# Performance work log

Measured on AMD Instinct MI355X. Metric: run time of the kernel, lower is better.

## Reference

```python
import jax, jax.numpy as jnp
import numpy as np

TEMP = 1.0
EPS = 1e-15

B, N, F, K = 8, 2000, 128, 64


def setup_inputs() -> dict:
    key = jax.random.key(0)
    k1, k2, k3 = jax.random.split(key, 3)
    x = jax.random.normal(k1, (B, N, F), dtype=jnp.float32)
    adj = jax.random.uniform(k2, (B, N, N), dtype=jnp.float32)
    s = jax.random.normal(k3, (B, N, K), dtype=jnp.float32)
    mask = jnp.ones((B, N), dtype=bool)
    return {"x": x, "adj": adj, "s": s, "mask": mask}


def reference(x, adj, s, mask):
    k = s.shape[-1]
    s = jax.nn.softmax(s / TEMP, axis=-1)
    m = mask[..., None].astype(x.dtype)          # [B,N,1]
    x = x * m
    s = s * m

    # pooled features: s^T x -> [B,K,F]
    out = jnp.einsum('bnk,bnf->bkf', s, x)

    # pooled adjacency: s^T A s -> [B,K,K]
    as_ = jnp.einsum('bnm,bmk->bnk', adj, s)     # A s, [B,N,K]
    out_adj = jnp.einsum('bnk,bnl->bkl', as_, s)

    # mincut loss
    mincut_num = jnp.einsum('bkk->b', out_adj)
    d_flat = jnp.sum(adj, axis=-1)               # degree, [B,N]
    # trace(s^T diag(d) s) = sum_n d_n * sum_k s_nk^2 (avoids dense diag)
    mincut_den = jnp.einsum('bn,bnk,bnk->b', d_flat, s, s)
    mincut_loss = jnp.mean(-(mincut_num / mincut_den))

    # orthogonality loss
    ss = jnp.einsum('bnk,bnl->bkl', s, s)        # [B,K,K]
    ss_norm = jnp.linalg.norm(ss, axis=(-2, -1), keepdims=True)
    i_s = jnp.eye(k, dtype=ss.dtype)
    ortho = jnp.linalg.norm(ss / ss_norm - i_s / jnp.sqrt(jnp.asarray(k, ss.dtype)), axis=(-2, -1))
    ortho_loss = jnp.mean(ortho)

    # zero diagonal, symmetric degree normalization
    ind = jnp.arange(k)
    out_adj = out_adj.at[:, ind, ind].set(0.0)
    d = jnp.sqrt(jnp.sum(out_adj, axis=-1))[:, None, :] + EPS  # [B,1,K]
    out_adj = out_adj / d / jnp.swapaxes(d, 1, 2)

    return out, out_adj, mincut_loss, ortho_loss
```

## Files before the change

### kernel.cpp

```cpp
#include <hip/hip_runtime.h>

typedef __bf16 bf16;
typedef __bf16 bf16x8 __attribute__((ext_vector_type(8)));
typedef float f32x4 __attribute__((ext_vector_type(4)));
typedef float f32x16 __attribute__((ext_vector_type(16)));

#define NB 8
#define NN 2000
#define N2 2048
#define KK 64
#define FF 128

__global__ __launch_bounds__(256) void k1_softmax(const float* __restrict__ s,
                                                  bf16* __restrict__ sT,
                                                  float* __restrict__ rowsq) {
  const int b = blockIdx.x >> 5, tile = blockIdx.x & 31;
  const int n0 = tile * 64;
  const int t = threadIdx.x;
  const int r = t >> 2, q = t & 3;
  __shared__ float ptile[64][65];
  const int n = n0 + r;
  const bool valid = n < NN;
  float v[16];
  if (valid) {
    const float4* src = (const float4*)(s + ((size_t)(b * NN + n)) * KK + q * 16);
#pragma unroll
    for (int i = 0; i < 4; ++i) {
      float4 f = src[i];
      v[4 * i + 0] = f.x; v[4 * i + 1] = f.y; v[4 * i + 2] = f.z; v[4 * i + 3] = f.w;
    }
  } else {
#pragma unroll
    for (int i = 0; i < 16; ++i) v[i] = 0.f;
  }
  float mx = v[0];
#pragma unroll
  for (int i = 1; i < 16; ++i) mx = fmaxf(mx, v[i]);
  mx = fmaxf(mx, __shfl_xor(mx, 1));
  mx = fmaxf(mx, __shfl_xor(mx, 2));
  float sum = 0.f;
#pragma unroll
  for (int i = 0; i < 16; ++i) { v[i] = __expf(v[i] - mx); sum += v[i]; }
  sum += __shfl_xor(sum, 1);
  sum += __shfl_xor(sum, 2);
  const float scale = valid ? (1.0f / sum) : 0.f;
  float rq = 0.f;
#pragma unroll
  for (int i = 0; i < 16; ++i) { v[i] *= scale; rq += v[i] * v[i]; }
  rq += __shfl_xor(rq, 1);
  rq += __shfl_xor(rq, 2);
  if (q == 0) rowsq[b * N2 + n0 + r] = rq;
#pragma unroll
  for (int i = 0; i < 16; ++i) ptile[r][q * 16 + i] = v[i];
  __syncthreads();
  bf16x8 o0, o1;
#pragma unroll
  for (int i = 0; i < 8; ++i) o0[i] = (bf16)ptile[q * 16 + i][r];
#pragma unroll
  for (int i = 0; i < 8; ++i) o1[i] = (bf16)ptile[q * 16 + 8 + i][r];
  bf16* dst = sT + ((size_t)(b * KK + r)) * N2 + n0 + q * 16;
  *(bf16x8*)dst = o0;
  *(bf16x8*)(dst + 8) = o1;
}

__global__ __launch_bounds__(256) void k1b_xt(const float* __restrict__ x,
                                              bf16* __restrict__ xT) {
  const int b = blockIdx.x >> 5, tile = blockIdx.x & 31;
  const int n0 = tile * 64;
  const int t = threadIdx.x;
  __shared__ float xt[64 * 132];
#pragma unroll
  for (int i = 0; i < 8; ++i) {
    int idx = t + 256 * i;
    int row = idx >> 5, c4 = idx & 31;
    int n = n0 + row;
    float4 vv = make_float4(0.f, 0.f, 0.f, 0.f);
    if (n < NN) vv = ((const float4*)(x + ((size_t)(b * NN + n)) * FF))[c4];
    *(float4*)&xt[row * 132 + c4 * 4] = vv;
  }
  __syncthreads();
  const int f = t >> 1, h = t & 1;
  bf16* dst = xT + ((size_t)(b * FF + f)) * N2 + n0 + h * 32;
#pragma unroll
  for (int g = 0; g < 4; ++g) {
    bf16x8 o;
#pragma unroll
    for (int i = 0; i < 8; ++i) o[i] = (bf16)xt[(h * 32 + g * 8 + i) * 132 + f];
    *(bf16x8*)(dst + g * 8) = o;
  }
}

__global__ __launch_bounds__(256) void k2_adjs(const float* __restrict__ adj,
                                               const bf16* __restrict__ sT,
                                               bf16* __restrict__ asT) {
  const int b = blockIdx.x >> 5, tile = blockIdx.x & 31;
  const int n0 = tile * 64;
  const int t = threadIdx.x;
  const int w = t >> 6, l = t & 63;
  const int lr = l & 15, lq = l >> 4;
  __shared__ bf16 aT[64 * 72];
  __shared__ bf16 sTl[64 * 72];
  f32x4 acc[4];
#pragma unroll
  for (int ct = 0; ct < 4; ++ct)
#pragma unroll
    for (int rr = 0; rr < 4; ++rr) acc[ct][rr] = 0.f;
  const int r = t >> 2, q = t & 3;
  const bool rowok = (n0 + r) < NN;
  const float* adjrow = adj + ((size_t)b * NN + (rowok ? (n0 + r) : 0)) * NN;
  const bf16* srow = sT + ((size_t)(b * KK + r)) * N2;
  for (int m0 = 0; m0 < N2; m0 += 64) {
    float fv[16];
#pragma unroll
    for (int i = 0; i < 4; ++i) {
      int m = m0 + q * 16 + i * 4;
      float4 f = make_float4(0.f, 0.f, 0.f, 0.f);
      if (rowok && m < NN) f = *(const float4*)(adjrow + m);
      fv[4 * i + 0] = f.x; fv[4 * i + 1] = f.y; fv[4 * i + 2] = f.z; fv[4 * i + 3] = f.w;
    }
    bf16x8 c0, c1;
#pragma unroll
    for (int i = 0; i < 8; ++i) { c0[i] = (bf16)fv[i]; c1[i] = (bf16)fv[8 + i]; }
    *(bf16x8*)&aT[r * 72 + q * 16] = c0;
    *(bf16x8*)&aT[r * 72 + q * 16 + 8] = c1;
    const bf16x8* sp = (const bf16x8*)(srow + m0 + q * 16);
    *(bf16x8*)&sTl[r * 72 + q * 16] = sp[0];
    *(bf16x8*)&sTl[r * 72 + q * 16 + 8] = sp[1];
    __syncthreads();
#pragma unroll
    for (int ks = 0; ks < 2; ++ks) {
      const int mo = ks * 32 + lq * 8;
      bf16x8 af = *(const bf16x8*)&aT[(w * 16 + lr) * 72 + mo];
#pragma unroll
      for (int ct = 0; ct < 4; ++ct) {
        bf16x8 bfv = *(const bf16x8*)&sTl[(ct * 16 + lr) * 72 + mo];
        acc[ct] = __builtin_amdgcn_mfma_f32_16x16x32_bf16(af, bfv, acc[ct], 0, 0, 0);
      }
    }
    __syncthreads();
  }
#pragma unroll
  for (int ct = 0; ct < 4; ++ct)
#pragma unroll
    for (int rr = 0; rr < 4; ++rr)
      aT[(ct * 16 + lr) * 72 + (w * 16 + lq * 4 + rr)] = (bf16)acc[ct][rr];
  __syncthreads();
  bf16* dst = asT + ((size_t)(b * KK + r)) * N2 + n0 + q * 16;
  *(bf16x8*)dst = *(const bf16x8*)&aT[r * 72 + q * 16];
  *(bf16x8*)(dst + 8) = *(const bf16x8*)&aT[r * 72 + q * 16 + 8];
}

__global__ __launch_bounds__(256) void k2b_den(const bf16* __restrict__ asT,
                                               const float* __restrict__ rowsq,
                                               float* __restrict__ den_part) {
  const int b = blockIdx.x >> 3, c = blockIdx.x & 7;
  const int t = threadIdx.x;
  const int n = c * 256 + t;
  const bf16* base = asT + (size_t)b * KK * N2 + n;
  float dsum = 0.f;
#pragma unroll 8
  for (int kk = 0; kk < KK; ++kk) dsum += (float)base[(size_t)kk * N2];
  float val = dsum * rowsq[b * N2 + n];
  __shared__ float red[256];
  red[t] = val;
  __syncthreads();
  for (int s2 = 128; s2 > 0; s2 >>= 1) {
    if (t < s2) red[t] += red[t + s2];
    __syncthreads();
  }
  if (t == 0) den_part[b * 8 + c] = red[0];
}

__global__ __launch_bounds__(256) void k3_gemms(const bf16* __restrict__ sT,
                                                const bf16* __restrict__ asT,
                                                const bf16* __restrict__ xT,
                                                float* __restrict__ adjraw,
                                                float* __restrict__ ssw,
                                                float* __restrict__ dout) {
  const int b = blockIdx.x >> 4, tile = blockIdx.x & 15;
  const bf16 *Ab, *Bb;
  float* Cb;
  int ldC, row0, col0;
  if (tile < 4) {
    int rt = tile >> 1, ct = tile & 1;
    Ab = asT + ((size_t)(b * KK + rt * 32)) * N2;
    Bb = sT + ((size_t)(b * KK + ct * 32)) * N2;
    Cb = adjraw + b * KK * KK; ldC = KK; row0 = rt * 32; col0 = ct * 32;
  } else if (tile < 8) {
    int u = tile - 4; int rt = u >> 1, ct = u & 1;
    Ab = sT + ((size_t)(b * KK + rt * 32)) * N2;
    Bb = sT + ((size_t)(b * KK + ct * 32)) * N2;
    Cb = ssw + b * KK * KK; ldC = KK; row0 = rt * 32; col0 = ct * 32;
  } else {
    int u = tile - 8; int rt = u >> 2, ct = u & 3;
    Ab = sT + ((size_t)(b * KK + rt * 32)) * N2;
    Bb = xT + ((size_t)(b * FF + ct * 32)) * N2;
    Cb = dout + b * KK * FF; ldC = FF; row0 = rt * 32; col0 = ct * 32;
  }
  const int t = threadIdx.x;
  const int w = t >> 6, l = t & 63;
  __shared__ bf16 At[32 * 72];
  __shared__ bf16 Bt[32 * 72];
  __shared__ float Ct[4 * 32 * 33];
  const int srow = t >> 3, sseg = t & 7;
  f32x16 acc;
#pragma unroll
  for (int i = 0; i < 16; ++i) acc[i] = 0.f;
  for (int m0 = 0; m0 < N2; m0 += 64) {
    *(bf16x8*)&At[srow * 72 + sseg * 8] = *(const bf16x8*)(Ab + (size_t)srow * N2 + m0 + sseg * 8);
    *(bf16x8*)&Bt[srow * 72 + sseg * 8] = *(const bf16x8*)(Bb + (size_t)srow * N2 + m0 + sseg * 8);
    __syncthreads();
    const int mo = w * 16 + (l >> 5) * 8;
    bf16x8 af = *(const bf16x8*)&At[(l & 31) * 72 + mo];
    bf16x8 bfv = *(const bf16x8*)&Bt[(l & 31) * 72 + mo];
    acc = __builtin_amdgcn_mfma_f32_32x32x16_bf16(af, bfv, acc, 0, 0, 0);
    __syncthreads();
  }
#pragma unroll
  for (int rr = 0; rr < 16; ++rr) {
    int row = (rr & 3) + 8 * (rr >> 2) + 4 * (l >> 5);
    Ct[(w * 32 + row) * 33 + (l & 31)] = acc[rr];
  }
  __syncthreads();
#pragma unroll
  for (int i = 0; i < 4; ++i) {
    int e = t + 256 * i;
    int row = e >> 5, col = e & 31;
    float v = Ct[row * 33 + col] + Ct[(32 + row) * 33 + col] +
              Ct[(64 + row) * 33 + col] + Ct[(96 + row) * 33 + col];
    Cb[(size_t)(row0 + row) * ldC + col0 + col] = v;
  }
}

__device__ inline float wred64(float v) {
#pragma unroll
  for (int off = 32; off > 0; off >>= 1) v += __shfl_xor(v, off);
  return v;
}

__global__ __launch_bounds__(64) void k4_final(const float* __restrict__ adjraw,
                                               const float* __restrict__ ssw,
                                               const float* __restrict__ den_part,
                                               float* __restrict__ dout,
                                               float* __restrict__ loss_part) {
  const int b = blockIdx.x;
  const int lane = threadIdx.x;
  float den = 0.f;
#pragma unroll
  for (int c = 0; c < 8; ++c) den += den_part[b * 8 + c];
  const float* arow = adjraw + b * 4096 + lane * 64;
  float4 av[16];
#pragma unroll
  for (int i = 0; i < 16; ++i) av[i] = ((const float4*)arow)[i];
  const float diag = adjraw[b * 4096 + lane * 65];
  float rs = 0.f;
#pragma unroll
  for (int i = 0; i < 16; ++i) rs += av[i].x + av[i].y + av[i].z + av[i].w;
  rs -= diag;
  const float num = wred64(diag);
  const float d = sqrtf(rs) + 1e-15f;
  __shared__ float dsh[64];
  dsh[lane] = d;
  __syncthreads();
  const float invd = 1.0f / d;
  float* orow = dout + NB * KK * FF + b * 4096 + lane * 64;
#pragma unroll
  for (int i = 0; i < 16; ++i) {
    float4 cvv = av[i];
    cvv.x = (4 * i + 0 == lane) ? 0.f : cvv.x * invd / dsh[4 * i + 0];
    cvv.y = (4 * i + 1 == lane) ? 0.f : cvv.y * invd / dsh[4 * i + 1];
    cvv.z = (4 * i + 2 == lane) ? 0.f : cvv.z * invd / dsh[4 * i + 2];
    cvv.w = (4 * i + 3 == lane) ? 0.f : cvv.w * invd / dsh[4 * i + 3];
    ((float4*)orow)[i] = cvv;
  }
  const float* srow = ssw + b * 4096 + lane * 64;
  float4 sv[16];
  float sq = 0.f;
#pragma unroll
  for (int i = 0; i < 16; ++i) {
    sv[i] = ((const float4*)srow)[i];
    sq += sv[i].x * sv[i].x + sv[i].y * sv[i].y + sv[i].z * sv[i].z + sv[i].w * sv[i].w;
  }
  const float frob = sqrtf(wred64(sq));
  const float fi = 1.0f / frob;
  float osum = 0.f;
#pragma unroll
  for (int i = 0; i < 16; ++i) {
    float tx = sv[i].x * fi - ((4 * i + 0 == lane) ? 0.125f : 0.f);
    float ty = sv[i].y * fi - ((4 * i + 1 == lane) ? 0.125f : 0.f);
    float tz = sv[i].z * fi - ((4 * i + 2 == lane) ? 0.125f : 0.f);
    float tw = sv[i].w * fi - ((4 * i + 3 == lane) ? 0.125f : 0.f);
    osum += tx * tx + ty * ty + tz * tz + tw * tw;
  }
  const float ot = wred64(osum);
  if (lane == 0) {
    loss_part[b] = -(num / den);
    loss_part[8 + b] = sqrtf(ot);
  }
}

__global__ void k5_loss(const float* __restrict__ loss_part, float* __restrict__ dout) {
  if (threadIdx.x == 0 && blockIdx.x == 0) {
    float m = 0.f, o = 0.f;
    for (int b2 = 0; b2 < 8; ++b2) { m += loss_part[b2]; o += loss_part[8 + b2]; }
    dout[NB * KK * FF + NB * KK * KK + 0] = m * 0.125f;
    dout[NB * KK * FF + NB * KK * KK + 1] = o * 0.125f;
  }
}

extern "C" void kernel_launch(void* const* d_in, const int* in_sizes, int n_in,
                              void* d_out, int out_size, void* d_ws, size_t ws_size,
                              hipStream_t stream) {
  const float* x = (const float*)d_in[0];
  const float* adj = (const float*)d_in[1];
  const float* s = (const float*)d_in[2];
  float* out = (float*)d_out;
  char* ws = (char*)d_ws;
  bf16* sT = (bf16*)ws;
  bf16* xT = (bf16*)(ws + (2u << 20));
  bf16* asT = (bf16*)(ws + (6u << 20));
  float* rowsq = (float*)(ws + (8u << 20));
  float* den_part = (float*)(ws + (8u << 20) + 65536);
  float* adjraw = (float*)(ws + (8u << 20) + 65536 + 1024);
  float* ssw = adjraw + NB * KK * KK;
  float* loss_part = ssw + NB * KK * KK;

  k1_softmax<<<256, 256, 0, stream>>>(s, sT, rowsq);
  k1b_xt<<<256, 256, 0, stream>>>(x, xT);
  k2_adjs<<<256, 256, 0, stream>>>(adj, sT, asT);
  k2b_den<<<64, 256, 0, stream>>>(asT, rowsq, den_part);
  k3_gemms<<<128, 256, 0, stream>>>(sT, asT, xT, adjraw, ssw, out);
  k4_final<<<8, 64, 0, stream>>>(adjraw, ssw, den_part, out, loss_part);
  k5_loss<<<1, 64, 0, stream>>>(loss_part, out);
}
```

Baseline: 255.5 us.

## Split adj·s GEMM over more blocks with split-K, fuse degree reduction

```diff
diff --git a/kernel.cpp b/kernel.cpp
--- a/kernel.cpp
+++ b/kernel.cpp
@@ -1,9 +1,9 @@
 #include <hip/hip_runtime.h>
 
 typedef __bf16 bf16;
+typedef __bf16 bf16x4 __attribute__((ext_vector_type(4)));
 typedef __bf16 bf16x8 __attribute__((ext_vector_type(8)));
 typedef float f32x4 __attribute__((ext_vector_type(4)));
-typedef float f32x16 __attribute__((ext_vector_type(16)));
 
 #define NB 8
 #define NN 2000
@@ -92,83 +92,81 @@
 
 __global__ __launch_bounds__(256) void k2_adjs(const float* __restrict__ adj,
                                                const bf16* __restrict__ sT,
-                                               bf16* __restrict__ asT) {
-  const int b = blockIdx.x >> 5, tile = blockIdx.x & 31;
-  const int n0 = tile * 64;
-  const int t = threadIdx.x;
-  const int w = t >> 6, l = t & 63;
-  const int lr = l & 15, lq = l >> 4;
-  __shared__ bf16 aT[64 * 72];
-  __shared__ bf16 sTl[64 * 72];
-  f32x4 acc[4];
-#pragma unroll
-  for (int ct = 0; ct < 4; ++ct)
-#pragma unroll
-    for (int rr = 0; rr < 4; ++rr) acc[ct][rr] = 0.f;
-  const int r = t >> 2, q = t & 3;
-  const bool rowok = (n0 + r) < NN;
-  const float* adjrow = adj + ((size_t)b * NN + (rowok ? (n0 + r) : 0)) * NN;
-  const bf16* srow = sT + ((size_t)(b * KK + r)) * N2;
-  for (int m0 = 0; m0 < N2; m0 += 64) {
-    float fv[16];
-#pragma unroll
-    for (int i = 0; i < 4; ++i) {
-      int m = m0 + q * 16 + i * 4;
-      float4 f = make_float4(0.f, 0.f, 0.f, 0.f);
-      if (rowok && m < NN) f = *(const float4*)(adjrow + m);
-      fv[4 * i + 0] = f.x; fv[4 * i + 1] = f.y; fv[4 * i + 2] = f.z; fv[4 * i + 3] = f.w;
-    }
-    bf16x8 c0, c1;
-#pragma unroll
-    for (int i = 0; i < 8; ++i) { c0[i] = (bf16)fv[i]; c1[i] = (bf16)fv[8 + i]; }
-    *(bf16x8*)&aT[r * 72 + q * 16] = c0;
-    *(bf16x8*)&aT[r * 72 + q * 16 + 8] = c1;
-    const bf16x8* sp = (const bf16x8*)(srow + m0 + q * 16);
-    *(bf16x8*)&sTl[r * 72 + q * 16] = sp[0];
-    *(bf16x8*)&sTl[r * 72 + q * 16 + 8] = sp[1];
-    __syncthreads();
-#pragma unroll
-    for (int ks = 0; ks < 2; ++ks) {
-      const int mo = ks * 32 + lq * 8;
-      bf16x8 af = *(const bf16x8*)&aT[(w * 16 + lr) * 72 + mo];
-#pragma unroll
-      for (int ct = 0; ct < 4; ++ct) {
-        bf16x8 bfv = *(const bf16x8*)&sTl[(ct * 16 + lr) * 72 + mo];
-        acc[ct] = __builtin_amdgcn_mfma_f32_16x16x32_bf16(af, bfv, acc[ct], 0, 0, 0);
-      }
-    }
-    __syncthreads();
-  }
-#pragma unroll
-  for (int ct = 0; ct < 4; ++ct)
-#pragma unroll
-    for (int rr = 0; rr < 4; ++rr)
-      aT[(ct * 16 + lr) * 72 + (w * 16 + lq * 4 + rr)] = (bf16)acc[ct][rr];
-  __syncthreads();
-  bf16* dst = asT + ((size_t)(b * KK + r)) * N2 + n0 + q * 16;
-  *(bf16x8*)dst = *(const bf16x8*)&aT[r * 72 + q * 16];
-  *(bf16x8*)(dst + 8) = *(const bf16x8*)&aT[r * 72 + q * 16 + 8];
-}
-
-__global__ __launch_bounds__(256) void k2b_den(const bf16* __restrict__ asT,
+                                               bf16* __restrict__ asT,
                                                const float* __restrict__ rowsq,
                                                float* __restrict__ den_part) {
-  const int b = blockIdx.x >> 3, c = blockIdx.x & 7;
+  const int b = blockIdx.x >> 7, tile = blockIdx.x & 127;
+  const int n0 = tile * 16;
   const int t = threadIdx.x;
-  const int n = c * 256 + t;
-  const bf16* base = asT + (size_t)b * KK * N2 + n;
+  if (n0 >= NN) {
+    if (t == 0) den_part[b * 128 + tile] = 0.f;
+    const int k = t >> 2, nseg = t & 3;
+    bf16x4 z = {(bf16)0.f, (bf16)0.f, (bf16)0.f, (bf16)0.f};
+    *(bf16x4*)(asT + ((size_t)(b * KK + k)) * N2 + n0 + nseg * 4) = z;
+    return;
+  }
+  const int w = t >> 6, l = t & 63;
+  const int lr = l & 15, lg = l >> 4;
+  const float* arow = adj + ((size_t)(b * NN + n0 + lr)) * NN;
+  const bf16* sbase = sT + (size_t)b * KK * N2;
+  f32x4 acc[4];
+#pragma unroll
+  for (int ct = 0; ct < 4; ++ct)
+#pragma unroll
+    for (int r = 0; r < 4; ++r) acc[ct][r] = 0.f;
+  const int m_begin = w * 512;
+#pragma unroll 4
+  for (int s = 0; s < 16; ++s) {
+    const int m0 = m_begin + s * 32;
+    int ma = m0 + lg * 8;
+    if (ma > NN - 8) ma = NN - 8;
+    const float4 a0 = *(const float4*)(arow + ma);
+    const float4 a1 = *(const float4*)(arow + ma + 4);
+    bf16x8 af;
+    af[0] = (bf16)a0.x; af[1] = (bf16)a0.y; af[2] = (bf16)a0.z; af[3] = (bf16)a0.w;
+    af[4] = (bf16)a1.x; af[5] = (bf16)a1.y; af[6] = (bf16)a1.z; af[7] = (bf16)a1.w;
+    const int mb = m0 + lg * 8;
+#pragma unroll
+    for (int ct = 0; ct < 4; ++ct) {
+      bf16x8 bfv = *(const bf16x8*)(sbase + (size_t)(ct * 16 + lr) * N2 + mb);
+      acc[ct] = __builtin_amdgcn_mfma_f32_16x16x32_bf16(af, bfv, acc[ct], 0, 0, 0);
+    }
+  }
+  __shared__ float red[4][16][64];
+  __shared__ float outv[16][64];
+  __shared__ float dnsh[16];
+#pragma unroll
+  for (int ct = 0; ct < 4; ++ct)
+#pragma unroll
+    for (int r = 0; r < 4; ++r)
+      red[w][lg * 4 + r][ct * 16 + lr] = acc[ct][r];
+  __syncthreads();
+  const int n = t >> 4, k4 = t & 15;
   float dsum = 0.f;
-#pragma unroll 8
-  for (int kk = 0; kk < KK; ++kk) dsum += (float)base[(size_t)kk * N2];
-  float val = dsum * rowsq[b * N2 + n];
-  __shared__ float red[256];
-  red[t] = val;
-  __syncthreads();
-  for (int s2 = 128; s2 > 0; s2 >>= 1) {
-    if (t < s2) red[t] += red[t + s2];
-    __syncthreads();
-  }
-  if (t == 0) den_part[b * 8 + c] = red[0];
+#pragma unroll
+  for (int j = 0; j < 4; ++j) {
+    const int kk = k4 * 4 + j;
+    const float v = red[0][n][kk] + red[1][n][kk] + red[2][n][kk] + red[3][n][kk];
+    outv[n][kk] = v;
+    dsum += v;
+  }
+  dsum += __shfl_xor(dsum, 1);
+  dsum += __shfl_xor(dsum, 2);
+  dsum += __shfl_xor(dsum, 4);
+  dsum += __shfl_xor(dsum, 8);
+  if (k4 == 0) dnsh[n] = dsum * rowsq[b * N2 + n0 + n];
+  __syncthreads();
+  if (t == 0) {
+    float dtot = 0.f;
+#pragma unroll
+    for (int i = 0; i < 16; ++i) dtot += dnsh[i];
+    den_part[b * 128 + tile] = dtot;
+  }
+  const int k = t >> 2, nseg = t & 3;
+  bf16x4 o;
+#pragma unroll
+  for (int j = 0; j < 4; ++j) o[j] = (bf16)outv[nseg * 4 + j][k];
+  *(bf16x4*)(asT + ((size_t)(b * KK + k)) * N2 + n0 + nseg * 4) = o;
 }
 
 __global__ __launch_bounds__(256) void k3_gemms(const bf16* __restrict__ sT,
@@ -177,59 +175,48 @@
                                                 float* __restrict__ adjraw,
                                                 float* __restrict__ ssw,
                                                 float* __restrict__ dout) {
-  const int b = blockIdx.x >> 4, tile = blockIdx.x & 15;
+  const int b = blockIdx.x >> 6, u = blockIdx.x & 63;
   const bf16 *Ab, *Bb;
   float* Cb;
-  int ldC, row0, col0;
-  if (tile < 4) {
-    int rt = tile >> 1, ct = tile & 1;
-    Ab = asT + ((size_t)(b * KK + rt * 32)) * N2;
-    Bb = sT + ((size_t)(b * KK + ct * 32)) * N2;
-    Cb = adjraw + b * KK * KK; ldC = KK; row0 = rt * 32; col0 = ct * 32;
-  } else if (tile < 8) {
-    int u = tile - 4; int rt = u >> 1, ct = u & 1;
-    Ab = sT + ((size_t)(b * KK + rt * 32)) * N2;
-    Bb = sT + ((size_t)(b * KK + ct * 32)) * N2;
-    Cb = ssw + b * KK * KK; ldC = KK; row0 = rt * 32; col0 = ct * 32;
+  int ldC;
+  if (u < 16) {
+    const int rt = u >> 2, ct = u & 3;
+    Ab = asT + ((size_t)(b * KK + rt * 16)) * N2;
+    Bb = sT + ((size_t)(b * KK + ct * 16)) * N2;
+    Cb = adjraw + b * KK * KK + rt * 16 * KK + ct * 16; ldC = KK;
+  } else if (u < 32) {
+    const int v = u - 16, rt = v >> 2, ct = v & 3;
+    Ab = sT + ((size_t)(b * KK + rt * 16)) * N2;
+    Bb = sT + ((size_t)(b * KK + ct * 16)) * N2;
+    Cb = ssw + b * KK * KK + rt * 16 * KK + ct * 16; ldC = KK;
   } else {
-    int u = tile - 8; int rt = u >> 2, ct = u & 3;
-    Ab = sT + ((size_t)(b * KK + rt * 32)) * N2;
-    Bb = xT + ((size_t)(b * FF + ct * 32)) * N2;
-    Cb = dout + b * KK * FF; ldC = FF; row0 = rt * 32; col0 = ct * 32;
+    const int v = u - 32, rt = v >> 3, ct = v & 7;
+    Ab = sT + ((size_t)(b * KK + rt * 16)) * N2;
+    Bb = xT + ((size_t)(b * FF + ct * 16)) * N2;
+    Cb = dout + b * KK * FF + rt * 16 * FF + ct * 16; ldC = FF;
   }
   const int t = threadIdx.x;
   const int w = t >> 6, l = t & 63;
-  __shared__ bf16 At[32 * 72];
-  __shared__ bf16 Bt[32 * 72];
-  __shared__ float Ct[4 * 32 * 33];
-  const int srow = t >> 3, sseg = t & 7;
-  f32x16 acc;
-#pragma unroll
-  for (int i = 0; i < 16; ++i) acc[i] = 0.f;
-  for (int m0 = 0; m0 < N2; m0 += 64) {
-    *(bf16x8*)&At[srow * 72 + sseg * 8] = *(const bf16x8*)(Ab + (size_t)srow * N2 + m0 + sseg * 8);
-    *(bf16x8*)&Bt[srow * 72 + sseg * 8] = *(const bf16x8*)(Bb + (size_t)srow * N2 + m0 + sseg * 8);
-    __syncthreads();
-    const int mo = w * 16 + (l >> 5) * 8;
-    bf16x8 af = *(const bf16x8*)&At[(l & 31) * 72 + mo];
-    bf16x8 bfv = *(const bf16x8*)&Bt[(l & 31) * 72 + mo];
-    acc = __builtin_amdgcn_mfma_f32_32x32x16_bf16(af, bfv, acc, 0, 0, 0);
-    __syncthreads();
-  }
-#pragma unroll
-  for (int rr = 0; rr < 16; ++rr) {
-    int row = (rr & 3) + 8 * (rr >> 2) + 4 * (l >> 5);
-    Ct[(w * 32 + row) * 33 + (l & 31)] = acc[rr];
-  }
-  __syncthreads();
-#pragma unroll
-  for (int i = 0; i < 4; ++i) {
-    int e = t + 256 * i;
-    int row = e >> 5, col = e & 31;
-    float v = Ct[row * 33 + col] + Ct[(32 + row) * 33 + col] +
-              Ct[(64 + row) * 33 + col] + Ct[(96 + row) * 33 + col];
-    Cb[(size_t)(row0 + row) * ldC + col0 + col] = v;
-  }
+  const int lr = l & 15, lg = l >> 4;
+  f32x4 acc;
+#pragma unroll
+  for (int r = 0; r < 4; ++r) acc[r] = 0.f;
+  const int m_begin = w * 512;
+#pragma unroll 4
+  for (int s = 0; s < 16; ++s) {
+    const int m = m_begin + s * 32 + lg * 8;
+    bf16x8 af = *(const bf16x8*)(Ab + (size_t)lr * N2 + m);
+    bf16x8 bfv = *(const bf16x8*)(Bb + (size_t)lr * N2 + m);
+    acc = __builtin_amdgcn_mfma_f32_16x16x32_bf16(af, bfv, acc, 0, 0, 0);
+  }
+  __shared__ float red[4][16][16];
+#pragma unroll
+  for (int r = 0; r < 4; ++r) red[w][lg * 4 + r][lr] = acc[r];
+  __syncthreads();
+  const int row = t >> 4, col = t & 15;
+  const float v = red[0][row][col] + red[1][row][col] +
+                  red[2][row][col] + red[3][row][col];
+  Cb[row * ldC + col] = v;
 }
 
 __device__ inline float wred64(float v) {
@@ -245,9 +232,8 @@
                                                float* __restrict__ loss_part) {
   const int b = blockIdx.x;
   const int lane = threadIdx.x;
-  float den = 0.f;
-#pragma unroll
-  for (int c = 0; c < 8; ++c) den += den_part[b * 8 + c];
+  const float dp = den_part[b * 128 + lane] + den_part[b * 128 + 64 + lane];
+  const float den = wred64(dp);
   const float* arow = adjraw + b * 4096 + lane * 64;
   float4 av[16];
 #pragma unroll
@@ -257,6 +243,7 @@
 #pragma unroll
   for (int i = 0; i < 16; ++i) rs += av[i].x + av[i].y + av[i].z + av[i].w;
   rs -= diag;
+  rs = fmaxf(rs, 0.f);
   const float num = wred64(diag);
   const float d = sqrtf(rs) + 1e-15f;
   __shared__ float dsh[64];
@@ -321,15 +308,14 @@
   bf16* asT = (bf16*)(ws + (6u << 20));
   float* rowsq = (float*)(ws + (8u << 20));
   float* den_part = (float*)(ws + (8u << 20) + 65536);
-  float* adjraw = (float*)(ws + (8u << 20) + 65536 + 1024);
+  float* adjraw = (float*)(ws + (8u << 20) + 65536 + 4096);
   float* ssw = adjraw + NB * KK * KK;
   float* loss_part = ssw + NB * KK * KK;
 
   k1_softmax<<<256, 256, 0, stream>>>(s, sT, rowsq);
   k1b_xt<<<256, 256, 0, stream>>>(x, xT);
-  k2_adjs<<<256, 256, 0, stream>>>(adj, sT, asT);
-  k2b_den<<<64, 256, 0, stream>>>(asT, rowsq, den_part);
-  k3_gemms<<<128, 256, 0, stream>>>(sT, asT, xT, adjraw, ssw, out);
+  k2_adjs<<<1024, 256, 0, stream>>>(adj, sT, asT, rowsq, den_part);
+  k3_gemms<<<512, 256, 0, stream>>>(sT, asT, xT, adjraw, ssw, out);
   k4_final<<<8, 64, 0, stream>>>(adjraw, ssw, den_part, out, loss_part);
   k5_loss<<<1, 64, 0, stream>>>(loss_part, out);
 }
```

Measured after the change: 244.3 us. 4.4% less time.
